# Kernel optimization log

Measured on AMD Instinct MI355X. Metric: run time of the kernel, lower is better.

Reference implementation:

```python
import jax, jax.numpy as jnp
import numpy as np

D = 64          # node_hidden_dim
MP_STEPS = 6    # num_step_message_passing
S2S_STEPS = 6   # num_step_set2set
LSTM_LAYERS = 3 # num_layer_set2set


def setup_inputs() -> dict:
    key = jax.random.key(0)
    ks = jax.random.split(key, 32)
    N, E, B = 10000, 50000, 500
    node_in, edge_in, edge_hid, out_dim = 15, 5, 128, 12
    s = 0.1
    inp = {}
    inp["node_feat"] = jax.random.normal(ks[0], (N, node_in), jnp.float32)
    inp["edge_feat"] = jax.random.normal(ks[1], (E, edge_in), jnp.float32)
    inp["src"] = jax.random.randint(ks[2], (E,), 0, N)
    inp["dst"] = jax.random.randint(ks[3], (E,), 0, N)
    inp["graph_ids"] = jnp.sort(jax.random.randint(ks[4], (N,), 0, B))
    inp["num_graphs"] = B
    # lin0
    inp["lin0_W"] = jax.random.normal(ks[5], (node_in, D), jnp.float32) * s
    inp["lin0_b"] = jnp.zeros((D,), jnp.float32)
    # edge network MLP (Linear -> ReLU -> Linear), output reshaped to D x D per edge
    inp["em_W1"] = jax.random.normal(ks[6], (edge_in, edge_hid), jnp.float32) * s
    inp["em_b1"] = jnp.zeros((edge_hid,), jnp.float32)
    inp["em_W2"] = jax.random.normal(ks[7], (edge_hid, D * D), jnp.float32) * 0.02
    inp["em_b2"] = jnp.zeros((D * D,), jnp.float32)
    inp["conv_bias"] = jnp.zeros((D,), jnp.float32)
    # GRU (input D, hidden D), torch layout: [3*D, in], gate order r,z,n
    inp["gru_Wih"] = jax.random.normal(ks[8], (3 * D, D), jnp.float32) * s
    inp["gru_Whh"] = jax.random.normal(ks[9], (3 * D, D), jnp.float32) * s
    inp["gru_bih"] = jnp.zeros((3 * D,), jnp.float32)
    inp["gru_bhh"] = jnp.zeros((3 * D,), jnp.float32)
    # Set2Set LSTM: input 2*D, hidden D, 3 layers. torch layout [4*D, in], gates i,f,g,o
    inp["lstm0_Wih"] = jax.random.normal(ks[10], (4 * D, 2 * D), jnp.float32) * s
    inp["lstm0_Whh"] = jax.random.normal(ks[11], (4 * D, D), jnp.float32) * s
    inp["lstm0_bih"] = jnp.zeros((4 * D,), jnp.float32)
    inp["lstm0_bhh"] = jnp.zeros((4 * D,), jnp.float32)
    inp["lstm12_Wih"] = jax.random.normal(ks[12], (2, 4 * D, D), jnp.float32) * s
    inp["lstm12_Whh"] = jax.random.normal(ks[13], (2, 4 * D, D), jnp.float32) * s
    inp["lstm12_bih"] = jnp.zeros((2, 4 * D), jnp.float32)
    inp["lstm12_bhh"] = jnp.zeros((2, 4 * D), jnp.float32)
    # output head
    inp["lin1_W"] = jax.random.normal(ks[14], (2 * D, D), jnp.float32) * s
    inp["lin1_b"] = jnp.zeros((D,), jnp.float32)
    inp["lin2_W"] = jax.random.normal(ks[15], (D, out_dim), jnp.float32) * s
    inp["lin2_b"] = jnp.zeros((out_dim,), jnp.float32)
    return inp


def _mpnn(node_feat, edge_feat, src, dst, graph_ids, num_graphs,
          lin0_W, lin0_b, em_W1, em_b1, em_W2, em_b2, conv_bias,
          gru_Wih, gru_Whh, gru_bih, gru_bhh,
          lstm0_Wih, lstm0_Whh, lstm0_bih, lstm0_bhh,
          lstm12_Wih, lstm12_Whh, lstm12_bih, lstm12_bhh,
          lin1_W, lin1_b, lin2_W, lin2_b):
    N = node_feat.shape[0]
    E = edge_feat.shape[0]
    B = num_graphs
    # initial node embedding
    out = jax.nn.relu(node_feat @ lin0_W + lin0_b)      # [N, D]
    h = out                                             # GRU hidden (seq_len=1, 1 layer)
    # per-edge weight matrices (edge features are static across steps)
    We = (jax.nn.relu(edge_feat @ em_W1 + em_b1) @ em_W2 + em_b2).reshape(E, D, D)
    for _ in range(MP_STEPS):
        # NNConv: gather src -> per-edge matvec -> scatter-add to dst
        msg = jnp.einsum('ei,eio->eo', out[src], We)    # [E, D]
        agg = jax.ops.segment_sum(msg, dst, num_segments=N) + conv_bias
        m = jax.nn.relu(agg)                            # [N, D]
        # GRU cell (torch gate order r, z, n)
        gx = m @ gru_Wih.T + gru_bih
        gh = h @ gru_Whh.T + gru_bhh
        rx, zx, nx = jnp.split(gx, 3, axis=-1)
        rh, zh, nh = jnp.split(gh, 3, axis=-1)
        r = jax.nn.sigmoid(rx + rh)
        z = jax.nn.sigmoid(zx + zh)
        n = jnp.tanh(nx + r * nh)
        h = (1.0 - z) * n + z * h
        out = h
    # Set2Set readout: 3-layer LSTM over steps, attention over nodes per graph
    h_l = [jnp.zeros((B, D), out.dtype) for _ in range(LSTM_LAYERS)]
    c_l = [jnp.zeros((B, D), out.dtype) for _ in range(LSTM_LAYERS)]
    q_star = jnp.zeros((B, 2 * D), out.dtype)
    for _ in range(S2S_STEPS):
        x = q_star
        for l in range(LSTM_LAYERS):
            if l == 0:
                Wih, Whh, bih, bhh = lstm0_Wih, lstm0_Whh, lstm0_bih, lstm0_bhh
            else:
                Wih, Whh = lstm12_Wih[l - 1], lstm12_Whh[l - 1]
                bih, bhh = lstm12_bih[l - 1], lstm12_bhh[l - 1]
            g = x @ Wih.T + bih + h_l[l] @ Whh.T + bhh
            i_g, f_g, g_g, o_g = jnp.split(g, 4, axis=-1)
            c_l[l] = jax.nn.sigmoid(f_g) * c_l[l] + jax.nn.sigmoid(i_g) * jnp.tanh(g_g)
            h_l[l] = jax.nn.sigmoid(o_g) * jnp.tanh(c_l[l])
            x = h_l[l]
        q = x                                           # [B, D]
        # segment softmax attention
        e = jnp.sum(out * q[graph_ids], axis=-1)        # [N]
        emax = jax.ops.segment_max(e, graph_ids, num_segments=B)
        ex = jnp.exp(e - emax[graph_ids])
        denom = jax.ops.segment_sum(ex, graph_ids, num_segments=B)
        alpha = ex / denom[graph_ids]                   # [N]
        readout = jax.ops.segment_sum(alpha[:, None] * out, graph_ids, num_segments=B)
        q_star = jnp.concatenate([q, readout], axis=-1) # [B, 2D]
    y = jax.nn.relu(q_star @ lin1_W + lin1_b) @ lin2_W + lin2_b
    return y


def reference(node_feat, edge_feat, src, dst, graph_ids, num_graphs,
              lin0_W, lin0_b, em_W1, em_b1, em_W2, em_b2, conv_bias,
              gru_Wih, gru_Whh, gru_bih, gru_bhh,
              lstm0_Wih, lstm0_Whh, lstm0_bih, lstm0_bhh,
              lstm12_Wih, lstm12_Whh, lstm12_bih, lstm12_bhh,
              lin1_W, lin1_b, lin2_W, lin2_b):
    return _mpnn(node_feat, edge_feat, src, dst, graph_ids, num_graphs,
                 lin0_W, lin0_b, em_W1, em_b1, em_W2, em_b2, conv_bias,
                 gru_Wih, gru_Whh, gru_bih, gru_bhh,
                 lstm0_Wih, lstm0_Whh, lstm0_bih, lstm0_bhh,
                 lstm12_Wih, lstm12_Whh, lstm12_bih, lstm12_bhh,
                 lin1_W, lin1_b, lin2_W, lin2_b)
```

## Files before the change

### kernel.cpp

```cpp
#include <hip/hip_runtime.h>
#include <math.h>

#define NGRAPH 500
#define MP_STEPS 6
#define S2S_STEPS 6

typedef _Float16 h8 __attribute__((ext_vector_type(8)));
typedef float f4 __attribute__((ext_vector_type(4)));

__device__ __forceinline__ float sigmoidf_(float v){ return 1.0f/(1.0f + expf(-v)); }

__global__ void k_zero(float* __restrict__ p, int n){
  int i = blockIdx.x*256 + threadIdx.x;
  if(i < n) p[i] = 0.f;
}

__global__ void k_lin0(const float* __restrict__ nf, const float* __restrict__ W,
                       const float* __restrict__ b, float* __restrict__ x, int N){
  int n = blockIdx.x*4 + (threadIdx.x >> 6);
  int d = threadIdx.x & 63;
  if(n >= N) return;
  float acc = b[d];
#pragma unroll
  for(int i=0;i<15;i++) acc = fmaf(nf[n*15+i], W[i*64+d], acc);
  x[n*64+d] = fmaxf(acc, 0.0f);
}

__global__ void k_edgeh(const float* __restrict__ ef, const float* __restrict__ W1,
                        const float* __restrict__ b1, _Float16* __restrict__ he, int E){
  int e = blockIdx.x;
  int h = threadIdx.x;
  if(e >= E || h >= 160) return;
  float v;
  if(h < 128){
    float acc = b1[h];
#pragma unroll
    for(int i=0;i<5;i++) acc = fmaf(ef[e*5+i], W1[i*128+h], acc);
    v = fmaxf(acc, 0.f);
  } else {
    v = (h == 128) ? 1.0f : 0.0f;
  }
  he[(size_t)e*160 + h] = (_Float16)v;
}

__global__ void k_prepW2(const float* __restrict__ W2, const float* __restrict__ b2,
                         _Float16* __restrict__ W2T){
  int idx = blockIdx.x*256 + threadIdx.x;
  if(idx >= 4096*160) return;
  int n = idx / 160, k = idx % 160;
  float v = (k < 128) ? W2[(size_t)k*4096 + n] : ((k == 128) ? b2[n] : 0.f);
  W2T[idx] = (_Float16)v;
}

__global__ __launch_bounds__(256, 2) void k_fmsg(
    const _Float16* __restrict__ he,
    const _Float16* __restrict__ W2T,
    const float* __restrict__ x,
    const int* __restrict__ src, const int* __restrict__ dst,
    float* __restrict__ agg, int E)
{
  __shared__ _Float16 hs[64*160];
  __shared__ float xsT[64*68];
  __shared__ int ds_dst[64];
  const int tid  = threadIdx.x;
  const int wave = tid >> 6;
  const int lane = tid & 63;
  const int quad = lane >> 4;
  const int l15  = lane & 15;
  const int e0   = blockIdx.x * 64;

  for(int t = tid; t < 1280; t += 256){
    int r = t / 20, c = t % 20;
    uint4 v = make_uint4(0,0,0,0);
    if(e0 + r < E) v = *(const uint4*)&he[(size_t)(e0+r)*160 + c*8];
    *(uint4*)&hs[r*160 + c*8] = v;
  }
  {
    int j = tid >> 2, qc = tid & 3;
    int sj = (e0 + j < E) ? src[e0 + j] : 0;
    const float4* xr = (const float4*)(x + (size_t)sj*64);
#pragma unroll
    for(int k=0;k<4;k++){
      float4 v = xr[qc*4 + k];
      int ib = qc*16 + k*4;
      xsT[(ib+0)*68 + j] = v.x;
      xsT[(ib+1)*68 + j] = v.y;
      xsT[(ib+2)*68 + j] = v.z;
      xsT[(ib+3)*68 + j] = v.w;
    }
  }
  if(tid < 64) ds_dst[tid] = (e0 + tid < E) ? dst[e0 + tid] : 0;
  __syncthreads();

  h8 af[4][5];
#pragma unroll
  for(int mt=0;mt<4;mt++)
#pragma unroll
    for(int ks=0;ks<5;ks++)
      af[mt][ks] = *(const h8*)&hs[(mt*16 + l15)*160 + ks*32 + (quad<<3)];

  const _Float16* bbase = W2T + ((size_t)(wave*16 + l15))*160 + (quad<<3);
  h8 bf[5], bn[5];
#pragma unroll
  for(int ks=0;ks<5;ks++) bf[ks] = *(const h8*)(bbase + ks*32);

  f4 macc[4];
#pragma unroll
  for(int mt=0;mt<4;mt++) macc[mt] = (f4){0.f,0.f,0.f,0.f};

#pragma unroll 2
  for(int i=0;i<64;i++){
    if(i < 63){
      const _Float16* nb = bbase + (size_t)(i+1)*64*160;
#pragma unroll
      for(int ks=0;ks<5;ks++) bn[ks] = *(const h8*)(nb + ks*32);
    }
    f4 g0 = (f4){0.f,0.f,0.f,0.f}, g1 = g0, g2 = g0, g3 = g0;
#pragma unroll
    for(int ks=0;ks<5;ks++){
      g0 = __builtin_amdgcn_mfma_f32_16x16x32_f16(af[0][ks], bf[ks], g0, 0, 0, 0);
      g1 = __builtin_amdgcn_mfma_f32_16x16x32_f16(af[1][ks], bf[ks], g1, 0, 0, 0);
      g2 = __builtin_amdgcn_mfma_f32_16x16x32_f16(af[2][ks], bf[ks], g2, 0, 0, 0);
      g3 = __builtin_amdgcn_mfma_f32_16x16x32_f16(af[3][ks], bf[ks], g3, 0, 0, 0);
    }
    f4 x0 = *(const f4*)&xsT[i*68 +  0 + (quad<<2)];
    f4 x1 = *(const f4*)&xsT[i*68 + 16 + (quad<<2)];
    f4 x2 = *(const f4*)&xsT[i*68 + 32 + (quad<<2)];
    f4 x3 = *(const f4*)&xsT[i*68 + 48 + (quad<<2)];
    macc[0] += x0 * g0;
    macc[1] += x1 * g1;
    macc[2] += x2 * g2;
    macc[3] += x3 * g3;
#pragma unroll
    for(int ks=0;ks<5;ks++) bf[ks] = bn[ks];
  }

  const int col = wave*16 + l15;
#pragma unroll
  for(int mt=0;mt<4;mt++){
#pragma unroll
    for(int r=0;r<4;r++){
      int edge = mt*16 + (quad<<2) + r;
      if(e0 + edge < E)
        atomicAdd(&agg[(size_t)ds_dst[edge]*64 + col], macc[mt][r]);
    }
  }
}

__global__ __launch_bounds__(256) void k_gru2(
    float* __restrict__ x, float* __restrict__ agg, const float* __restrict__ cb,
    const float* __restrict__ WihT, const float* __restrict__ WhhT,
    const float* __restrict__ bih, const float* __restrict__ bhh, int N)
{
  __shared__ float ms[32*64], hs2[32*64];
  const int tid = threadIdx.x;
  const int n0 = blockIdx.x*32;
  for(int t=tid; t<2048; t+=256){
    int n = n0 + (t>>6), d = t&63;
    float mv=0.f, hv=0.f;
    if(n < N){
      mv = fmaxf(agg[(size_t)n*64+d] + cb[d], 0.f);
      agg[(size_t)n*64+d] = 0.f;
      hv = x[(size_t)n*64+d];
    }
    ms[t]=mv; hs2[t]=hv;
  }
  __syncthreads();
  const int gx = tid & 31, ng = tid >> 5;
  float ar[4][2]={{0}}, az[4][2]={{0}}, anx[4][2]={{0}}, anh[4][2]={{0}};
  for(int k=0;k<64;k++){
    float wi0=WihT[k*192+gx],     wi1=WihT[k*192+gx+32];
    float wi2=WihT[k*192+gx+64],  wi3=WihT[k*192+gx+96];
    float wi4=WihT[k*192+gx+128], wi5=WihT[k*192+gx+160];
    float wh0=WhhT[k*192+gx],     wh1=WhhT[k*192+gx+32];
    float wh2=WhhT[k*192+gx+64],  wh3=WhhT[k*192+gx+96];
    float wh4=WhhT[k*192+gx+128], wh5=WhhT[k*192+gx+160];
#pragma unroll
    for(int j=0;j<4;j++){
      float mk = ms[(ng*4+j)*64+k], hk = hs2[(ng*4+j)*64+k];
      ar[j][0] = fmaf(mk,wi0, fmaf(hk,wh0, ar[j][0]));
      ar[j][1] = fmaf(mk,wi1, fmaf(hk,wh1, ar[j][1]));
      az[j][0] = fmaf(mk,wi2, fmaf(hk,wh2, az[j][0]));
      az[j][1] = fmaf(mk,wi3, fmaf(hk,wh3, az[j][1]));
      anx[j][0]= fmaf(mk,wi4, anx[j][0]);
      anx[j][1]= fmaf(mk,wi5, anx[j][1]);
      anh[j][0]= fmaf(hk,wh4, anh[j][0]);
      anh[j][1]= fmaf(hk,wh5, anh[j][1]);
    }
  }
#pragma unroll
  for(int j=0;j<4;j++){
    int n = n0 + ng*4 + j;
    if(n >= N) continue;
#pragma unroll
    for(int c=0;c<2;c++){
      int d = gx + 32*c;
      float r  = sigmoidf_(ar[j][c] + bih[d]     + bhh[d]);
      float z  = sigmoidf_(az[j][c] + bih[64+d]  + bhh[64+d]);
      float nn = tanhf(anx[j][c] + bih[128+d] + r*(anh[j][c] + bhh[128+d]));
      float hv = hs2[(ng*4+j)*64+d];
      x[(size_t)n*64+d] = (1.f - z)*nn + z*hv;
    }
  }
}

__global__ void k_tr_gru(const float* __restrict__ Wih, const float* __restrict__ Whh,
                         float* __restrict__ WihT, float* __restrict__ WhhT){
  int idx = blockIdx.x*256 + threadIdx.x;
  if(idx < 192*64){
    int r = idx/64, i = idx%64;
    WihT[i*192 + r] = Wih[idx];
    WhhT[i*192 + r] = Whh[idx];
  }
}

__global__ void k_tr_lstm(const float* __restrict__ w0ih, const float* __restrict__ w0hh,
                          const float* __restrict__ w12ih, const float* __restrict__ w12hh,
                          float* __restrict__ t0ih, float* __restrict__ t0hh,
                          float* __restrict__ t12ih, float* __restrict__ t12hh){
  int idx = blockIdx.x*256 + threadIdx.x;
  if(idx < 256*128){ int r = idx/128, k = idx%128; t0ih[k*256+r] = w0ih[idx]; }
  if(idx < 256*64){ int r = idx/64, k = idx%64; t0hh[k*256+r] = w0hh[idx]; }
  if(idx < 2*256*64){
    int l = idx/(256*64); int rem = idx%(256*64); int r = rem/64, k = rem%64;
    t12ih[l*64*256 + k*256 + r] = w12ih[idx];
    t12hh[l*64*256 + k*256 + r] = w12hh[idx];
  }
}

__device__ __forceinline__ int lbound(const int* __restrict__ a, int n, int v){
  int lo=0, hi=n;
  while(lo<hi){ int mid=(lo+hi)>>1; if(a[mid]<v) lo=mid+1; else hi=mid; }
  return lo;
}

__global__ __launch_bounds__(256) void k_s2s(
    const float* __restrict__ x, const int* __restrict__ gid, int N,
    const float* __restrict__ t0ih, const float* __restrict__ t0hh,
    const float* __restrict__ l0_bih, const float* __restrict__ l0_bhh,
    const float* __restrict__ t12ih, const float* __restrict__ t12hh,
    const float* __restrict__ l12_bih, const float* __restrict__ l12_bhh,
    const float* __restrict__ W1, const float* __restrict__ b1,
    const float* __restrict__ W2, const float* __restrict__ b2,
    float* __restrict__ y)
{
  const int b = blockIdx.x;
  const int t = threadIdx.x;
  const int wave = t >> 6, lane = t & 63;
  __shared__ float hsl[3][64], csl[3][64], qs[128], gs[256];
  __shared__ float rop[4*64], wred[4], wsum[4];
  __shared__ int sh_n0, sh_n1;

  if(t == 0) sh_n0 = lbound(gid, N, b);
  if(t == 1) sh_n1 = lbound(gid, N, b+1);
  if(t < 192){ hsl[t>>6][t&63] = 0.f; csl[t>>6][t&63] = 0.f; }
  if(t < 128) qs[t] = 0.f;
  __syncthreads();
  const int n0 = sh_n0, cnt = sh_n1 - sh_n0;

  for(int step=0; step<S2S_STEPS; step++){
#pragma unroll
    for(int l=0; l<3; l++){
      const float* Wih; const float* Whh; const float* bi; const float* bh;
      const float* xin; int in_dim;
      if(l == 0){ Wih=t0ih; Whh=t0hh; bi=l0_bih; bh=l0_bhh; xin=qs; in_dim=128; }
      else { Wih = t12ih + (l-1)*64*256; Whh = t12hh + (l-1)*64*256;
             bi = l12_bih + (l-1)*256;  bh = l12_bhh + (l-1)*256;
             xin = hsl[l-1]; in_dim = 64; }
      float g = bi[t] + bh[t];
      for(int k=0;k<in_dim;k++) g = fmaf(xin[k], Wih[k*256+t], g);
      for(int k=0;k<64;k++)     g = fmaf(hsl[l][k], Whh[k*256+t], g);
      gs[t] = g;
      __syncthreads();
      if(t < 64){
        float ig = sigmoidf_(gs[t]);
        float fg = sigmoidf_(gs[64+t]);
        float gg = tanhf(gs[128+t]);
        float og = sigmoidf_(gs[192+t]);
        float cn = fg*csl[l][t] + ig*gg;
        csl[l][t] = cn;
        hsl[l][t] = og*tanhf(cn);
      }
      __syncthreads();
    }
    float qv = hsl[2][lane];
    float pm = -1e30f;
    for(int j = wave; j < cnt; j += 4){
      float p = x[(size_t)(n0+j)*64 + lane] * qv;
#pragma unroll
      for(int o=32;o;o>>=1) p += __shfl_xor(p, o, 64);
      pm = fmaxf(pm, p);
    }
    if(lane == 0) wred[wave] = pm;
    __syncthreads();
    float mx = fmaxf(fmaxf(wred[0],wred[1]), fmaxf(wred[2],wred[3]));
    float pro = 0.f, ps = 0.f;
    for(int j = wave; j < cnt; j += 4){
      float p = x[(size_t)(n0+j)*64 + lane] * qv;
#pragma unroll
      for(int o=32;o;o>>=1) p += __shfl_xor(p, o, 64);
      float ex = expf(p - mx);
      ps += ex;
      pro = fmaf(ex, x[(size_t)(n0+j)*64 + lane], pro);
    }
    rop[wave*64 + lane] = pro;
    if(lane == 0) wsum[wave] = ps;
    __syncthreads();
    if(t < 64){
      float tot = wsum[0]+wsum[1]+wsum[2]+wsum[3];
      float inv = (tot > 0.f) ? 1.f/tot : 0.f;
      float rv = (rop[t] + rop[64+t] + rop[128+t] + rop[192+t]) * inv;
      qs[t] = hsl[2][t];
      qs[64+t] = rv;
    }
    __syncthreads();
  }
  if(t < 64){
    float a = b1[t];
    for(int k=0;k<128;k++) a = fmaf(qs[k], W1[k*64+t], a);
    gs[t] = fmaxf(a, 0.f);
  }
  __syncthreads();
  if(t < 12){
    float o = b2[t];
    for(int k=0;k<64;k++) o = fmaf(gs[k], W2[k*12+t], o);
    y[b*12+t] = o;
  }
}

extern "C" void kernel_launch(void* const* d_in, const int* in_sizes, int n_in,
                              void* d_out, int out_size, void* d_ws, size_t ws_size,
                              hipStream_t stream) {
  const float* node_feat = (const float*)d_in[0];
  const float* edge_feat = (const float*)d_in[1];
  const int*   src       = (const int*)d_in[2];
  const int*   dst       = (const int*)d_in[3];
  const int*   gid       = (const int*)d_in[4];
  const float* lin0_W = (const float*)d_in[6];
  const float* lin0_b = (const float*)d_in[7];
  const float* em_W1  = (const float*)d_in[8];
  const float* em_b1  = (const float*)d_in[9];
  const float* em_W2  = (const float*)d_in[10];
  const float* em_b2  = (const float*)d_in[11];
  const float* conv_b = (const float*)d_in[12];
  const float* gru_Wih = (const float*)d_in[13];
  const float* gru_Whh = (const float*)d_in[14];
  const float* gru_bih = (const float*)d_in[15];
  const float* gru_bhh = (const float*)d_in[16];
  const float* l0_Wih = (const float*)d_in[17];
  const float* l0_Whh = (const float*)d_in[18];
  const float* l0_bih = (const float*)d_in[19];
  const float* l0_bhh = (const float*)d_in[20];
  const float* l12_Wih = (const float*)d_in[21];
  const float* l12_Whh = (const float*)d_in[22];
  const float* l12_bih = (const float*)d_in[23];
  const float* l12_bhh = (const float*)d_in[24];
  const float* lin1_W = (const float*)d_in[25];
  const float* lin1_b = (const float*)d_in[26];
  const float* lin2_W = (const float*)d_in[27];
  const float* lin2_b = (const float*)d_in[28];
  float* y = (float*)d_out;

  const int N = in_sizes[0] / 15;
  const int E = in_sizes[1] / 5;
  const int B = NGRAPH;

  char* p = (char*)d_ws;
  auto carve = [&](size_t bytes)->char* {
    char* r = p; p += (bytes + 255) & ~(size_t)255; return r;
  };
  _Float16* he_h = (_Float16*)carve((size_t)E*160*2);
  _Float16* W2T  = (_Float16*)carve((size_t)4096*160*2);
  float* x     = (float*)carve((size_t)N*64*4);
  float* agg   = (float*)carve((size_t)N*64*4);
  float* gWihT = (float*)carve(192*64*4);
  float* gWhhT = (float*)carve(192*64*4);
  float* t0ih  = (float*)carve(128*256*4);
  float* t0hh  = (float*)carve(64*256*4);
  float* t12ih = (float*)carve(2*64*256*4);
  float* t12hh = (float*)carve(2*64*256*4);
  (void)ws_size; (void)n_in; (void)out_size;

  k_lin0<<<(N+3)/4, 256, 0, stream>>>(node_feat, lin0_W, lin0_b, x, N);
  k_edgeh<<<E, 192, 0, stream>>>(edge_feat, em_W1, em_b1, he_h, E);
  k_prepW2<<<(4096*160+255)/256, 256, 0, stream>>>(em_W2, em_b2, W2T);
  k_tr_gru<<<(192*64+255)/256, 256, 0, stream>>>(gru_Wih, gru_Whh, gWihT, gWhhT);
  k_tr_lstm<<<(2*256*64+255)/256, 256, 0, stream>>>(l0_Wih, l0_Whh, l12_Wih, l12_Whh,
                                                    t0ih, t0hh, t12ih, t12hh);
  k_zero<<<(N*64+255)/256, 256, 0, stream>>>(agg, N*64);

  const int nblk = (E + 63) / 64;
  for(int s=0; s<MP_STEPS; s++){
    k_fmsg<<<nblk, 256, 0, stream>>>(he_h, W2T, x, src, dst, agg, E);
    k_gru2<<<(N+31)/32, 256, 0, stream>>>(x, agg, conv_b, gWihT, gWhhT, gru_bih, gru_bhh, N);
  }

  k_s2s<<<B, 256, 0, stream>>>(x, gid, N,
                               t0ih, t0hh, l0_bih, l0_bhh,
                               t12ih, t12hh, l12_bih, l12_bhh,
                               lin1_W, lin1_b, lin2_W, lin2_b, y);
}
```

Baseline: 1.101 ms.

## Cache graph node features in LDS for Set2Set and raise fmsg occupancy

The Set2Set kernel now stages each graph's node features (up to 128 nodes) in shared memory once and caches the attention scores, so the second softmax pass no longer recomputes dot products or rereads global memory. Nodes beyond the cap fall back to the old global path. The LSTM layers become a templated helper with four-way split accumulators and compile-time input size, and several loops get unroll pragmas. The fmsg kernel's launch bounds raise the occupancy hint from 2 to 4 blocks per CU, which may force register spills.

```diff
diff --git a/kernel.cpp b/kernel.cpp
--- a/kernel.cpp
+++ b/kernel.cpp
@@ -4,6 +4,7 @@
 #define NGRAPH 500
 #define MP_STEPS 6
 #define S2S_STEPS 6
+#define S2S_CAP 128
 
 typedef _Float16 h8 __attribute__((ext_vector_type(8)));
 typedef float f4 __attribute__((ext_vector_type(4)));
@@ -52,7 +53,7 @@
   W2T[idx] = (_Float16)v;
 }
 
-__global__ __launch_bounds__(256, 2) void k_fmsg(
+__global__ __launch_bounds__(256, 4) void k_fmsg(
     const _Float16* __restrict__ he,
     const _Float16* __restrict__ W2T,
     const float* __restrict__ x,
@@ -168,6 +169,7 @@
   __syncthreads();
   const int gx = tid & 31, ng = tid >> 5;
   float ar[4][2]={{0}}, az[4][2]={{0}}, anx[4][2]={{0}}, anh[4][2]={{0}};
+#pragma unroll 4
   for(int k=0;k<64;k++){
     float wi0=WihT[k*192+gx],     wi1=WihT[k*192+gx+32];
     float wi2=WihT[k*192+gx+64],  wi3=WihT[k*192+gx+96];
@@ -232,6 +234,42 @@
   int lo=0, hi=n;
   while(lo<hi){ int mid=(lo+hi)>>1; if(a[mid]<v) lo=mid+1; else hi=mid; }
   return lo;
+}
+
+template<int IN>
+__device__ __forceinline__ void lstm_layer(
+    const float* __restrict__ xin, float* __restrict__ hv, float* __restrict__ cv,
+    const float* __restrict__ WihT, const float* __restrict__ WhhT,
+    const float* __restrict__ bi, const float* __restrict__ bh,
+    float* __restrict__ gs, int t)
+{
+  float a0=0.f,a1=0.f,a2=0.f,a3=0.f;
+#pragma unroll
+  for(int k=0;k<IN;k+=4){
+    a0 = fmaf(xin[k+0], WihT[(k+0)*256+t], a0);
+    a1 = fmaf(xin[k+1], WihT[(k+1)*256+t], a1);
+    a2 = fmaf(xin[k+2], WihT[(k+2)*256+t], a2);
+    a3 = fmaf(xin[k+3], WihT[(k+3)*256+t], a3);
+  }
+#pragma unroll
+  for(int k=0;k<64;k+=4){
+    a0 = fmaf(hv[k+0], WhhT[(k+0)*256+t], a0);
+    a1 = fmaf(hv[k+1], WhhT[(k+1)*256+t], a1);
+    a2 = fmaf(hv[k+2], WhhT[(k+2)*256+t], a2);
+    a3 = fmaf(hv[k+3], WhhT[(k+3)*256+t], a3);
+  }
+  gs[t] = (a0+a1)+(a2+a3) + bi[t] + bh[t];
+  __syncthreads();
+  if(t < 64){
+    float ig = sigmoidf_(gs[t]);
+    float fg = sigmoidf_(gs[64+t]);
+    float gg = tanhf(gs[128+t]);
+    float og = sigmoidf_(gs[192+t]);
+    float cn = fg*cv[t] + ig*gg;
+    cv[t] = cn;
+    hv[t] = og*tanhf(cn);
+  }
+  __syncthreads();
 }
 
 __global__ __launch_bounds__(256) void k_s2s(
@@ -247,8 +285,9 @@
   const int b = blockIdx.x;
   const int t = threadIdx.x;
   const int wave = t >> 6, lane = t & 63;
+  __shared__ float xt[S2S_CAP*64];
   __shared__ float hsl[3][64], csl[3][64], qs[128], gs[256];
-  __shared__ float rop[4*64], wred[4], wsum[4];
+  __shared__ float ps[S2S_CAP], rop[4*64], wred[4], wsum[4];
   __shared__ int sh_n0, sh_n1;
 
   if(t == 0) sh_n0 = lbound(gid, N, b);
@@ -257,35 +296,27 @@
   if(t < 128) qs[t] = 0.f;
   __syncthreads();
   const int n0 = sh_n0, cnt = sh_n1 - sh_n0;
+  const int cc = (cnt < S2S_CAP) ? cnt : S2S_CAP;
+
+  for(int j = wave; j < cc; j += 4)
+    xt[j*64 + lane] = x[(size_t)(n0+j)*64 + lane];
+  __syncthreads();
 
   for(int step=0; step<S2S_STEPS; step++){
-#pragma unroll
-    for(int l=0; l<3; l++){
-      const float* Wih; const float* Whh; const float* bi; const float* bh;
-      const float* xin; int in_dim;
-      if(l == 0){ Wih=t0ih; Whh=t0hh; bi=l0_bih; bh=l0_bhh; xin=qs; in_dim=128; }
-      else { Wih = t12ih + (l-1)*64*256; Whh = t12hh + (l-1)*64*256;
-             bi = l12_bih + (l-1)*256;  bh = l12_bhh + (l-1)*256;
-             xin = hsl[l-1]; in_dim = 64; }
-      float g = bi[t] + bh[t];
-      for(int k=0;k<in_dim;k++) g = fmaf(xin[k], Wih[k*256+t], g);
-      for(int k=0;k<64;k++)     g = fmaf(hsl[l][k], Whh[k*256+t], g);
-      gs[t] = g;
-      __syncthreads();
-      if(t < 64){
-        float ig = sigmoidf_(gs[t]);
-        float fg = sigmoidf_(gs[64+t]);
-        float gg = tanhf(gs[128+t]);
-        float og = sigmoidf_(gs[192+t]);
-        float cn = fg*csl[l][t] + ig*gg;
-        csl[l][t] = cn;
-        hsl[l][t] = og*tanhf(cn);
-      }
-      __syncthreads();
-    }
+    lstm_layer<128>(qs,     hsl[0], csl[0], t0ih,           t0hh,           l0_bih,        l0_bhh,        gs, t);
+    lstm_layer<64>(hsl[0],  hsl[1], csl[1], t12ih,          t12hh,          l12_bih,       l12_bhh,       gs, t);
+    lstm_layer<64>(hsl[1],  hsl[2], csl[2], t12ih + 64*256, t12hh + 64*256, l12_bih + 256, l12_bhh + 256, gs, t);
+
     float qv = hsl[2][lane];
     float pm = -1e30f;
-    for(int j = wave; j < cnt; j += 4){
+    for(int j = wave; j < cc; j += 4){
+      float p = xt[j*64 + lane] * qv;
+#pragma unroll
+      for(int o=32;o;o>>=1) p += __shfl_xor(p, o, 64);
+      if(lane == 0) ps[j] = p;
+      pm = fmaxf(pm, p);
+    }
+    for(int j = S2S_CAP + wave; j < cnt; j += 4){
       float p = x[(size_t)(n0+j)*64 + lane] * qv;
 #pragma unroll
       for(int o=32;o;o>>=1) p += __shfl_xor(p, o, 64);
@@ -294,17 +325,24 @@
     if(lane == 0) wred[wave] = pm;
     __syncthreads();
     float mx = fmaxf(fmaxf(wred[0],wred[1]), fmaxf(wred[2],wred[3]));
-    float pro = 0.f, ps = 0.f;
-    for(int j = wave; j < cnt; j += 4){
-      float p = x[(size_t)(n0+j)*64 + lane] * qv;
+
+    float pro = 0.f, pssum = 0.f;
+    for(int j = wave; j < cc; j += 4){
+      float ex = expf(ps[j] - mx);
+      pssum += ex;
+      pro = fmaf(ex, xt[j*64 + lane], pro);
+    }
+    for(int j = S2S_CAP + wave; j < cnt; j += 4){
+      float xv = x[(size_t)(n0+j)*64 + lane];
+      float p = xv * qv;
 #pragma unroll
       for(int o=32;o;o>>=1) p += __shfl_xor(p, o, 64);
       float ex = expf(p - mx);
-      ps += ex;
-      pro = fmaf(ex, x[(size_t)(n0+j)*64 + lane], pro);
+      pssum += ex;
+      pro = fmaf(ex, xv, pro);
     }
     rop[wave*64 + lane] = pro;
-    if(lane == 0) wsum[wave] = ps;
+    if(lane == 0) wsum[wave] = pssum;
     __syncthreads();
     if(t < 64){
       float tot = wsum[0]+wsum[1]+wsum[2]+wsum[3];
@@ -317,12 +355,14 @@
   }
   if(t < 64){
     float a = b1[t];
+#pragma unroll 4
     for(int k=0;k<128;k++) a = fmaf(qs[k], W1[k*64+t], a);
     gs[t] = fmaxf(a, 0.f);
   }
   __syncthreads();
   if(t < 12){
     float o = b2[t];
+#pragma unroll 4
     for(int k=0;k<64;k++) o = fmaf(gs[k], W2[k*12+t], o);
     y[b*12+t] = o;
   }
```

New measurement: 3.262 ms. 2.96x slower.
